# Performance work log

Hardware: AMD Instinct MI355X
Metric: run time of the kernel (lower is better)

## Reference

```python
import jax, jax.numpy as jnp
import numpy as np

# Hard-coded 36-node detector graph from the source (1-indexed), 220 directed edges.
E_SRC = [1,2,3,4,5,6,7,8,9,10,11,12,13,14,15,16,17,18,19,20,21,22,23,24,25,26,27,28,29,30,31,32,33,34,35,36,4,3,8,7,19,20,15,16,35,36,31,32,11,12,11,11,11,12,12,12,6,5,25,26,28,25,9,9,9,10,10,10,1,2,3,4,5,6,7,8,9,10,11,12,13,14,15,16,17,18,17,18,19,20,16,15,31,32,36,35,3,4,7,8,6,5,25,28,14,9,12,11,1,4,2,3,4,1,6,7,8,5,10,11,12,9,14,15,16,13,18,19,20,17,22,23,24,21,26,27,28,25,30,31,32,29,34,35,36,33,33,34,1,2,14,13,30,29,23,22,21,24,22,21,36,33,4,31,30,15,27,28,18,17,10,9,14,19,18,5,8,1,19,20,21,22,23,24,25,26,27,28,29,30,31,32,33,34,35,36,25,26,13,14,30,29,24,21,23,22,33,34,1,2,28,27,10,9,12,15,22,21,11,10]
E_DST = [2,3,4,1,6,7,8,5,10,11,12,9,14,15,16,13,18,19,20,17,22,23,24,21,26,27,28,25,30,31,32,29,34,35,36,33,33,34,1,2,14,13,30,29,23,22,21,24,22,21,36,33,4,31,30,15,27,28,18,17,10,9,14,19,18,5,8,1,19,20,21,22,23,24,25,26,27,28,29,30,31,32,33,34,35,36,25,26,13,14,30,29,24,21,23,22,33,34,1,2,28,27,10,9,12,15,22,21,11,10,1,2,3,4,5,6,7,8,9,10,11,12,13,14,15,16,17,18,19,20,21,22,23,24,25,26,27,28,29,30,31,32,33,34,35,36,4,3,8,7,19,20,15,16,35,36,31,32,11,12,11,11,11,12,12,12,6,5,25,26,28,25,9,9,9,10,10,10,1,2,3,4,5,6,7,8,9,10,11,12,13,14,15,16,17,18,17,18,19,20,16,15,31,32,36,35,3,4,7,8,6,5,25,28,14,9,12,11,1,4]

B = 20000   # graphs per batch
P = 36      # nodes per graph
N = B * P


def setup_inputs() -> dict:
    key = jax.random.key(0)
    ks = jax.random.split(key, 12)
    src = np.asarray(E_SRC, np.int32) - 1
    dst = np.asarray(E_DST, np.int32) - 1
    offs = (np.arange(B, dtype=np.int32) * P)[:, None]
    edge_index = jnp.asarray(np.stack([(src[None, :] + offs).reshape(-1),
                                       (dst[None, :] + offs).reshape(-1)]))  # [2, B*220]
    batch_index = jnp.asarray(np.repeat(np.arange(B, dtype=np.int32), P))  # [N]
    x = jax.random.normal(ks[0], (N, 2), jnp.float32)
    pos = jax.random.normal(ks[1], (N, 3), jnp.float32)  # unused by forward (faithful to source)

    def lin_w(k, fi, fo):
        s = 1.0 / np.sqrt(fi)
        return jax.random.uniform(k, (fi, fo), jnp.float32, -s, s)

    def lin_b(k, fo):
        return jax.random.uniform(k, (fo,), jnp.float32, -0.05, 0.05)

    return {
        "x": x, "edge_index": edge_index, "pos": pos, "batch_index": batch_index,
        "W0": lin_w(ks[2], 2, 4),   "b0": lin_b(ks[3], 4),
        "W1": lin_w(ks[4], 4, 12),  "b1": lin_b(ks[5], 12),
        "W2": lin_w(ks[6], 12, 16), "b2": lin_b(ks[7], 16),
        "W3": lin_w(ks[8], 16, 32), "b3": lin_b(ks[9], 32),
        "Wfc": lin_w(ks[10], 64, 7), "bfc": lin_b(ks[11], 7),
    }


def reference(x, edge_index, pos, batch_index, W0, b0, W1, b1, W2, b2, W3, b3, Wfc, bfc):
    del pos  # present in the torch signature but unused
    src, dst = edge_index[0], edge_index[1]
    n = x.shape[0]
    # GCN symmetric normalization with self-loops: deg = 1 + in-degree
    deg = jax.ops.segment_sum(jnp.ones(src.shape, x.dtype), dst, num_segments=n) + 1.0
    inv = deg ** -0.5
    enorm = inv[src] * inv[dst]   # edge norm
    snorm = inv * inv             # self-loop norm (deg^-1)

    def gcn_conv(h, W, b):
        h = h @ W  # [n, fo]
        agg = jax.ops.segment_sum(h[src] * enorm[:, None], dst, num_segments=n)
        return agg + h * snorm[:, None] + b

    h = jax.nn.relu(gcn_conv(x, W0, b0))
    h = jax.nn.relu(gcn_conv(h, W1, b1))
    # dropout(0.2) is identity in eval mode
    h = jax.nn.relu(gcn_conv(h, W2, b2))
    h = jax.nn.relu(gcn_conv(h, W3, b3))

    gmp = jax.ops.segment_max(h, batch_index, num_segments=B)
    counts = jax.ops.segment_sum(jnp.ones((n,), h.dtype), batch_index, num_segments=B)
    gap = jax.ops.segment_sum(h, batch_index, num_segments=B) / counts[:, None]
    hidden = jnp.concatenate([gmp, gap], axis=1)  # [B, 64]
    out = jax.nn.relu(hidden @ Wfc + bfc)         # [B, 7]
    return (out, hidden)
```

## Files before the change

kernel.cpp:

```cpp
#include <hip/hip_runtime.h>

typedef __attribute__((ext_vector_type(2))) float f32x2;
typedef __attribute__((ext_vector_type(4))) float f32x4;
typedef _Float16 f16;
typedef __attribute__((ext_vector_type(4))) _Float16 f16x4;
typedef __attribute__((ext_vector_type(8))) _Float16 f16x8;

#define NGRAPH 20000
#define GPB 7
#define STRIDE 36
#define SB (STRIDE * 4)

static __constant__ int c_indeg[36] = {
    7,5,5,7,6,5,5,6,9,9,9,9,5,7,7,5,5,6,6,5,7,7,5,5,7,5,5,7,5,6,6,5,6,5,5,6
};
static __constant__ signed char c_adj[36][9] = {
    {3,7,9,6,1,18,10,0,0},      {0,6,7,2,19,0,0,0,0},
    {1,3,33,32,20,0,0,0,0},     {2,10,0,32,21,33,9,0,0},
    {7,9,5,27,22,26,0,0,0},     {4,6,26,23,27,0,0,0,0},
    {5,7,1,24,0,0,0,0,0},       {6,9,4,0,25,1,0,0,0},
    {11,24,27,9,13,18,17,26,14},{8,27,24,3,10,4,7,0,27},
    {9,0,11,21,35,32,3,28,20},  {10,13,8,20,30,29,14,29,21},
    {15,19,18,13,30,0,0,0,0},   {12,18,8,19,14,31,11,0,0},
    {13,11,8,15,29,32,28,0,0},  {14,12,28,33,29,0,0,0,0},
    {19,25,17,34,24,0,0,0,0},   {16,24,8,18,35,25,0,0,0},
    {17,8,0,19,13,12,0,0,0},    {18,1,16,12,13,0,0,0,0},
    {23,30,11,2,31,10,21,0,0},  {20,35,10,3,34,11,22,0,0},
    {21,34,4,35,23,0,0,0,0},    {22,31,5,30,20,0,0,0,0},
    {27,6,16,25,17,8,9,0,0},    {24,7,17,26,16,0,0,0,0},
    {25,5,8,27,4,0,0,0,0},      {26,4,9,5,24,9,8,0,0},
    {31,15,10,14,29,0,0,0,0},   {28,14,11,11,15,30,0,0,0},
    {29,11,12,31,20,23,0,0,0},  {30,13,28,23,20,0,0,0,0},
    {35,3,10,14,2,33,0,0,0},    {32,2,15,3,34,0,0,0,0},
    {33,16,35,22,21,0,0,0,0},   {34,10,17,32,21,22,0,0,0},
};
static __constant__ float c_inv[36] = {
    0.35355339f,0.40824829f,0.40824829f,0.35355339f,0.37796447f,0.40824829f,
    0.40824829f,0.37796447f,0.31622777f,0.31622777f,0.31622777f,0.31622777f,
    0.40824829f,0.35355339f,0.35355339f,0.40824829f,0.40824829f,0.37796447f,
    0.37796447f,0.40824829f,0.35355339f,0.35355339f,0.40824829f,0.40824829f,
    0.35355339f,0.40824829f,0.40824829f,0.35355339f,0.40824829f,0.37796447f,
    0.37796447f,0.40824829f,0.37796447f,0.40824829f,0.40824829f,0.37796447f,
};
#define A_ 0.35355339f
#define B_ 0.40824829f
#define C_ 0.37796447f
#define D_ 0.31622777f
static __constant__ float c_ninv[36][9] = {
    {A_,C_,D_,B_,B_,C_,D_,0,0}, {A_,B_,C_,B_,B_,0,0,0,0},
    {B_,A_,B_,C_,A_,0,0,0,0},   {B_,D_,A_,C_,A_,B_,D_,0,0},
    {C_,D_,B_,A_,B_,B_,0,0,0},  {C_,B_,B_,B_,A_,0,0,0,0},
    {B_,C_,B_,A_,A_,0,0,0,0},   {B_,D_,C_,A_,B_,B_,0,0,0},
    {D_,A_,A_,D_,A_,C_,C_,B_,A_},{D_,A_,A_,A_,D_,C_,C_,A_,A_},
    {D_,A_,D_,A_,C_,C_,A_,B_,A_},{D_,A_,D_,A_,C_,C_,A_,C_,A_},
    {B_,B_,C_,A_,C_,0,0,0,0},   {B_,C_,D_,B_,A_,B_,D_,0,0},
    {A_,D_,D_,B_,C_,C_,B_,0,0}, {A_,B_,B_,B_,C_,0,0,0,0},
    {B_,B_,C_,B_,A_,0,0,0,0},   {B_,A_,D_,C_,C_,B_,0,0,0},
    {C_,D_,A_,B_,A_,B_,0,0,0},  {C_,B_,B_,B_,A_,0,0,0,0},
    {B_,C_,D_,B_,B_,D_,A_,0,0}, {A_,C_,D_,A_,B_,D_,B_,0,0},
    {A_,B_,C_,C_,B_,0,0,0,0},   {B_,B_,B_,C_,A_,0,0,0,0},
    {A_,B_,B_,B_,C_,D_,D_,0,0}, {A_,C_,C_,B_,B_,0,0,0,0},
    {B_,B_,D_,A_,C_,0,0,0,0},   {B_,C_,D_,B_,A_,D_,D_,0,0},
    {B_,B_,D_,A_,C_,0,0,0,0},   {B_,A_,D_,D_,B_,C_,0,0,0},
    {C_,D_,B_,B_,A_,B_,0,0,0},  {C_,A_,B_,B_,A_,0,0,0,0},
    {C_,A_,D_,A_,B_,B_,0,0,0},  {C_,B_,B_,A_,B_,0,0,0,0},
    {B_,B_,C_,B_,A_,0,0,0,0},   {B_,D_,C_,C_,A_,B_,0,0,0},
};

static __device__ __forceinline__ f32x2 relu2(f32x2 v) {
    return __builtin_elementwise_max(v, (f32x2){0.f, 0.f});
}

extern "C" __global__ __launch_bounds__(256, 4)
void gcn_fused(const float* __restrict__ x,
               const float* __restrict__ W0, const float* __restrict__ b0,
               const float* __restrict__ W1, const float* __restrict__ b1,
               const float* __restrict__ W2, const float* __restrict__ b2,
               const float* __restrict__ W3, const float* __restrict__ b3,
               const float* __restrict__ Wfc, const float* __restrict__ bfc,
               float* __restrict__ out)
{
    __shared__ float L[GPB * 36 * STRIDE];

    const int t = threadIdx.x;
    const int g = t / 36;
    const int v = t - g * 36;
    const bool act = (g < GPB);
    const int gq = act ? g : GPB - 1;
    const int vc = act ? v : 0;
    const int G  = blockIdx.x * GPB + g;
    const int Gc = (act && G < NGRAPH) ? G : 0;

    const int nd = c_indeg[vc];
    const float inv_v = c_inv[vc];
    const float* nr = &c_ninv[vc][0];
    int aoff[9];
#pragma unroll
    for (int k = 0; k < 9; ++k)
        aoff[k] = (gq * 36 + (int)c_adj[vc][k]) * SB;
    float* srow = &L[(gq * 36 + vc) * STRIDE];
    char* srowb = (char*)srow;
    const char* Lb = (const char*)L;

    f32x2 h0a, h0b;
    {
        const float2 xv = ((const float2*)x)[(size_t)Gc * 36 + vc];
        const float s0 = xv.x * inv_v, s1 = xv.y * inv_v;
        if (act) { srow[32] = s0; srow[33] = s1; }
        __syncthreads();
        f32x2 c = {s0, s1};
#pragma unroll
        for (int k = 0; k < 5; ++k) c += *(const f32x2*)(Lb + aoff[k] + 128);
        if (nd > 5) c += *(const f32x2*)(Lb + aoff[5] + 128);
        if (nd > 6) c += *(const f32x2*)(Lb + aoff[6] + 128);
        if (nd > 7) { c += *(const f32x2*)(Lb + aoff[7] + 128);
                      c += *(const f32x2*)(Lb + aoff[8] + 128); }
        const float a0 = c.x * inv_v, a1 = c.y * inv_v;
        const f32x2 a0v = {a0, a0}, a1v = {a1, a1};
        const f32x2* W0v = (const f32x2*)W0;
        const f32x2* b0v = (const f32x2*)b0;
        h0a = relu2(__builtin_elementwise_fma(a0v, W0v[0],
                    __builtin_elementwise_fma(a1v, W0v[2], b0v[0])));
        h0b = relu2(__builtin_elementwise_fma(a0v, W0v[1],
                    __builtin_elementwise_fma(a1v, W0v[3], b0v[1])));
    }

    f32x2 h1[6];
    {
        const f32x2 iv = {inv_v, inv_v};
        const f32x2 s0 = h0a * iv, s1 = h0b * iv;
        if (act) *(f32x4*)&srow[0] = (f32x4){s0.x, s0.y, s1.x, s1.y};
        __syncthreads();
        f32x4 c = {s0.x, s0.y, s1.x, s1.y};
#pragma unroll
        for (int k = 0; k < 5; ++k) c += *(const f32x4*)(Lb + aoff[k]);
        if (nd > 5) c += *(const f32x4*)(Lb + aoff[5]);
        if (nd > 6) c += *(const f32x4*)(Lb + aoff[6]);
        if (nd > 7) { c += *(const f32x4*)(Lb + aoff[7]);
                      c += *(const f32x4*)(Lb + aoff[8]); }
        float a[4];
#pragma unroll
        for (int i = 0; i < 4; ++i) a[i] = c[i] * inv_v;
        f32x2 z[6];
        const f32x2* b1v = (const f32x2*)b1;
#pragma unroll
        for (int j = 0; j < 6; ++j) z[j] = b1v[j];
        const f32x2* W1v = (const f32x2*)W1;
#pragma unroll
        for (int i = 0; i < 4; ++i) {
            const f32x2 av = {a[i], a[i]};
#pragma unroll
            for (int j = 0; j < 6; ++j)
                z[j] = __builtin_elementwise_fma(av, W1v[i * 6 + j], z[j]);
        }
#pragma unroll
        for (int j = 0; j < 6; ++j) h1[j] = relu2(z[j]);
    }

    f32x2 h2[8];
    {
        if (act) {
            f16x8 wlo; f16x4 whi;
#pragma unroll
            for (int j = 0; j < 4; ++j) {
                wlo[2*j]   = (f16)h1[j].x;
                wlo[2*j+1] = (f16)h1[j].y;
            }
#pragma unroll
            for (int j = 0; j < 2; ++j) {
                whi[2*j]   = (f16)h1[4+j].x;
                whi[2*j+1] = (f16)h1[4+j].y;
            }
            *(f16x8*)(srowb + 16) = wlo;
            *(f16x4*)(srowb + 32) = whi;
        }
        __syncthreads();
        float c[12];
#pragma unroll
        for (int j = 0; j < 6; ++j) {
            c[2*j]   = h1[j].x * inv_v;
            c[2*j+1] = h1[j].y * inv_v;
        }
#pragma unroll
        for (int k = 0; k < 9; ++k) {
            if (k >= 5) {
                if (k == 5 && nd <= 5) break;
                if (k == 6 && nd <= 6) break;
                if (k == 7 && nd <= 7) break;
            }
            const char* base = Lb + aoff[k];
            const f16x8 lo = *(const f16x8*)(base + 16);
            const f16x4 hi = *(const f16x4*)(base + 32);
            const float w = nr[k];
#pragma unroll
            for (int i = 0; i < 8; ++i) c[i]     = fmaf((float)lo[i], w, c[i]);
#pragma unroll
            for (int i = 0; i < 4; ++i) c[8 + i] = fmaf((float)hi[i], w, c[8 + i]);
        }
        float a[12];
#pragma unroll
        for (int i = 0; i < 12; ++i) a[i] = c[i] * inv_v;
        f32x2 z[8];
        const f32x2* b2v = (const f32x2*)b2;
#pragma unroll
        for (int j = 0; j < 8; ++j) z[j] = b2v[j];
        const f32x2* W2v = (const f32x2*)W2;
#pragma unroll
        for (int i = 0; i < 12; ++i) {
            const f32x2 av = {a[i], a[i]};
#pragma unroll
            for (int j = 0; j < 8; ++j)
                z[j] = __builtin_elementwise_fma(av, W2v[i * 8 + j], z[j]);
        }
#pragma unroll
        for (int j = 0; j < 8; ++j) h2[j] = relu2(z[j]);
    }

    f32x2 h3[16];
    {
        if (act) {
            f16x8 wlo, whi;
#pragma unroll
            for (int j = 0; j < 4; ++j) {
                wlo[2*j]   = (f16)h2[j].x;
                wlo[2*j+1] = (f16)h2[j].y;
                whi[2*j]   = (f16)h2[4+j].x;
                whi[2*j+1] = (f16)h2[4+j].y;
            }
            *(f16x8*)(srowb + 48) = wlo;
            *(f16x8*)(srowb + 64) = whi;
        }
        __syncthreads();
        float c[16];
#pragma unroll
        for (int j = 0; j < 8; ++j) {
            c[2*j]   = h2[j].x * inv_v;
            c[2*j+1] = h2[j].y * inv_v;
        }
#pragma unroll
        for (int k = 0; k < 9; ++k) {
            if (k >= 5) {
                if (k == 5 && nd <= 5) break;
                if (k == 6 && nd <= 6) break;
                if (k == 7 && nd <= 7) break;
            }
            const char* base = Lb + aoff[k];
            const f16x8 lo = *(const f16x8*)(base + 48);
            const f16x8 hi = *(const f16x8*)(base + 64);
            const float w = nr[k];
#pragma unroll
            for (int i = 0; i < 8; ++i) c[i]     = fmaf((float)lo[i], w, c[i]);
#pragma unroll
            for (int i = 0; i < 8; ++i) c[8 + i] = fmaf((float)hi[i], w, c[8 + i]);
        }
        float a[16];
#pragma unroll
        for (int i = 0; i < 16; ++i) a[i] = c[i] * inv_v;
        f32x2 z[16];
        const f32x2* b3v = (const f32x2*)b3;
#pragma unroll
        for (int j = 0; j < 16; ++j) z[j] = b3v[j];
        const f32x2* W3v = (const f32x2*)W3;
#pragma unroll
        for (int i = 0; i < 16; ++i) {
            const f32x2 av = {a[i], a[i]};
#pragma unroll
            for (int j = 0; j < 16; ++j)
                z[j] = __builtin_elementwise_fma(av, W3v[i * 16 + j], z[j]);
        }
#pragma unroll
        for (int j = 0; j < 16; ++j) h3[j] = relu2(z[j]);
    }

    if (act) {
        *(f32x4*)&srow[0] = (f32x4){h3[0].x, h3[0].y, h3[1].x, h3[1].y};
        *(f32x4*)&srow[4] = (f32x4){h3[2].x, h3[2].y, h3[3].x, h3[3].y};
        *(f32x4*)&srow[8] = (f32x4){h3[4].x, h3[4].y, h3[5].x, h3[5].y};
    }
    __syncthreads();
    if (act) {
#pragma unroll
        for (int q = 0; q < 5; ++q)
            *(f32x4*)&srow[12 + q * 4] =
                (f32x4){h3[6+2*q].x, h3[6+2*q].y, h3[7+2*q].x, h3[7+2*q].y};
    }
    __syncthreads();

    if (t < GPB * 32) {
        const int pg = t >> 5, pf = t & 31;
        const int PG = blockIdx.x * GPB + pg;
        const float* col = &L[(pg * 36) * STRIDE + pf];
        float mx = -1e30f, sm = 0.f;
#pragma unroll
        for (int u = 0; u < 36; ++u) {
            const float val = col[u * STRIDE];
            mx = fmaxf(mx, val); sm += val;
        }
        const float gap = sm * (1.0f / 36.0f);
        if (PG < NGRAPH) {
            float* ho = out + (size_t)NGRAPH * 7 + (size_t)PG * 64;
            ho[pf] = mx; ho[32 + pf] = gap;
        }
        float p[7];
        const float* wr0 = Wfc + pf * 7;
        const float* wr1 = Wfc + (32 + pf) * 7;
#pragma unroll
        for (int o = 0; o < 7; ++o)
            p[o] = fmaf(mx, wr0[o], gap * wr1[o]);
#pragma unroll
        for (int m = 16; m >= 1; m >>= 1) {
#pragma unroll
            for (int o = 0; o < 7; ++o)
                p[o] += __shfl_xor(p[o], m, 32);
        }
        if (pf < 7 && PG < NGRAPH) {
            float w = p[0];
            w = (pf == 1) ? p[1] : w;
            w = (pf == 2) ? p[2] : w;
            w = (pf == 3) ? p[3] : w;
            w = (pf == 4) ? p[4] : w;
            w = (pf == 5) ? p[5] : w;
            w = (pf == 6) ? p[6] : w;
            out[(size_t)PG * 7 + pf] = fmaxf(w + bfc[pf], 0.f);
        }
    }
}

extern "C" void kernel_launch(void* const* d_in, const int* in_sizes, int n_in,
                              void* d_out, int out_size, void* d_ws, size_t ws_size,
                              hipStream_t stream) {
    (void)in_sizes; (void)n_in; (void)d_ws; (void)ws_size; (void)out_size;
    const float* x   = (const float*)d_in[0];
    const float* W0  = (const float*)d_in[4];
    const float* b0  = (const float*)d_in[5];
    const float* W1  = (const float*)d_in[6];
    const float* b1  = (const float*)d_in[7];
    const float* W2  = (const float*)d_in[8];
    const float* b2  = (const float*)d_in[9];
    const float* W3  = (const float*)d_in[10];
    const float* b3  = (const float*)d_in[11];
    const float* Wfc = (const float*)d_in[12];
    const float* bfc = (const float*)d_in[13];
    float* out = (float*)d_out;

    const int nblocks = (NGRAPH + GPB - 1) / GPB;
    hipLaunchKernelGGL(gcn_fused, dim3(nblocks), dim3(256), 0, stream,
                       x, W0, b0, W1, b1, W2, b2, W3, b3, Wfc, bfc, out);
}
```

Before: 36.64 us.

## Gather layer-0 inputs from global memory, unroll aggregation, use LDS-based FC head

Layer 0 now reads neighbor features directly from global x instead of staging them in shared memory, which removes one barrier. Adjacency bytes are unpacked from packed words. The per-layer aggregation loops are replaced with explicit macro expansions guarded by in-degree. The final FC head is changed from a 7-way shuffle reduction to a staging pass: pooled features go to a small LDS region and 49 threads each compute one output dot product. This adds one barrier and extra LDS but removes the shuffle traffic.

```diff
diff --git a/kernel.cpp b/kernel.cpp
--- a/kernel.cpp
+++ b/kernel.cpp
@@ -10,6 +10,8 @@
 #define GPB 7
 #define STRIDE 36
 #define SB (STRIDE * 4)
+#define HID_OFF (GPB * 36 * STRIDE)
+#define HSTR 68
 
 static __constant__ int c_indeg[36] = {
     7,5,5,7,6,5,5,6,9,9,9,9,5,7,7,5,5,6,6,5,7,7,5,5,7,5,5,7,5,6,6,5,6,5,5,6
@@ -80,7 +82,7 @@
                const float* __restrict__ Wfc, const float* __restrict__ bfc,
                float* __restrict__ out)
 {
-    __shared__ float L[GPB * 36 * STRIDE];
+    __shared__ float L[GPB * 36 * STRIDE + GPB * HSTR];
 
     const int t = threadIdx.x;
     const int g = t / 36;
@@ -94,28 +96,47 @@
     const int nd = c_indeg[vc];
     const float inv_v = c_inv[vc];
     const float* nr = &c_ninv[vc][0];
-    int aoff[9];
-#pragma unroll
-    for (int k = 0; k < 9; ++k)
-        aoff[k] = (gq * 36 + (int)c_adj[vc][k]) * SB;
+    int nb[9], aoff[9];
+    {
+        const unsigned char* ar = (const unsigned char*)&c_adj[vc][0];
+        const unsigned int w0 = *(const unsigned int*)(ar);
+        const unsigned int w1 = *(const unsigned int*)(ar + 4);
+        const unsigned int w2 = *(const unsigned int*)(ar + 8);
+#pragma unroll
+        for (int k = 0; k < 4; ++k) nb[k] = (int)((w0 >> (8 * k)) & 0xff);
+#pragma unroll
+        for (int k = 0; k < 4; ++k) nb[4 + k] = (int)((w1 >> (8 * k)) & 0xff);
+        nb[8] = (int)(w2 & 0xff);
+#pragma unroll
+        for (int k = 0; k < 9; ++k) aoff[k] = (gq * 36 + nb[k]) * SB;
+    }
     float* srow = &L[(gq * 36 + vc) * STRIDE];
     char* srowb = (char*)srow;
     const char* Lb = (const char*)L;
 
     f32x2 h0a, h0b;
     {
-        const float2 xv = ((const float2*)x)[(size_t)Gc * 36 + vc];
-        const float s0 = xv.x * inv_v, s1 = xv.y * inv_v;
-        if (act) { srow[32] = s0; srow[33] = s1; }
-        __syncthreads();
-        f32x2 c = {s0, s1};
-#pragma unroll
-        for (int k = 0; k < 5; ++k) c += *(const f32x2*)(Lb + aoff[k] + 128);
-        if (nd > 5) c += *(const f32x2*)(Lb + aoff[5] + 128);
-        if (nd > 6) c += *(const f32x2*)(Lb + aoff[6] + 128);
-        if (nd > 7) { c += *(const f32x2*)(Lb + aoff[7] + 128);
-                      c += *(const f32x2*)(Lb + aoff[8] + 128); }
-        const float a0 = c.x * inv_v, a1 = c.y * inv_v;
+        const float2* x2 = (const float2*)x;
+        const int xb = Gc * 36;
+        const float2 xs = x2[xb + vc];
+        f32x2 acc = {xs.x * inv_v, xs.y * inv_v};
+#pragma unroll
+        for (int k = 0; k < 5; ++k) {
+            const float2 xu = x2[xb + nb[k]];
+            const float w = nr[k];
+            acc.x = fmaf(w, xu.x, acc.x); acc.y = fmaf(w, xu.y, acc.y);
+        }
+        if (nd > 5) { const float2 xu = x2[xb + nb[5]]; const float w = nr[5];
+            acc.x = fmaf(w, xu.x, acc.x); acc.y = fmaf(w, xu.y, acc.y); }
+        if (nd > 6) { const float2 xu = x2[xb + nb[6]]; const float w = nr[6];
+            acc.x = fmaf(w, xu.x, acc.x); acc.y = fmaf(w, xu.y, acc.y); }
+        if (nd > 7) {
+            const float2 xu7 = x2[xb + nb[7]]; const float w7 = nr[7];
+            acc.x = fmaf(w7, xu7.x, acc.x); acc.y = fmaf(w7, xu7.y, acc.y);
+            const float2 xu8 = x2[xb + nb[8]]; const float w8 = nr[8];
+            acc.x = fmaf(w8, xu8.x, acc.x); acc.y = fmaf(w8, xu8.y, acc.y);
+        }
+        const float a0 = acc.x * inv_v, a1 = acc.y * inv_v;
         const f32x2 a0v = {a0, a0}, a1v = {a1, a1};
         const f32x2* W0v = (const f32x2*)W0;
         const f32x2* b0v = (const f32x2*)b0;
@@ -181,22 +202,19 @@
             c[2*j]   = h1[j].x * inv_v;
             c[2*j+1] = h1[j].y * inv_v;
         }
-#pragma unroll
-        for (int k = 0; k < 9; ++k) {
-            if (k >= 5) {
-                if (k == 5 && nd <= 5) break;
-                if (k == 6 && nd <= 6) break;
-                if (k == 7 && nd <= 7) break;
-            }
-            const char* base = Lb + aoff[k];
-            const f16x8 lo = *(const f16x8*)(base + 16);
-            const f16x4 hi = *(const f16x4*)(base + 32);
-            const float w = nr[k];
-#pragma unroll
-            for (int i = 0; i < 8; ++i) c[i]     = fmaf((float)lo[i], w, c[i]);
-#pragma unroll
-            for (int i = 0; i < 4; ++i) c[8 + i] = fmaf((float)hi[i], w, c[8 + i]);
-        }
+#define AGG2(K) { const char* base = Lb + aoff[K];                              \
+        const f16x8 lo = *(const f16x8*)(base + 16);                            \
+        const f16x4 hi = *(const f16x4*)(base + 32);                            \
+        const float w = nr[K];                                                  \
+        _Pragma("unroll") for (int i = 0; i < 8; ++i)                           \
+            c[i] = fmaf((float)lo[i], w, c[i]);                                 \
+        _Pragma("unroll") for (int i = 0; i < 4; ++i)                           \
+            c[8+i] = fmaf((float)hi[i], w, c[8+i]); }
+        AGG2(0) AGG2(1) AGG2(2) AGG2(3) AGG2(4)
+        if (nd > 5) AGG2(5)
+        if (nd > 6) AGG2(6)
+        if (nd > 7) { AGG2(7) AGG2(8) }
+#undef AGG2
         float a[12];
 #pragma unroll
         for (int i = 0; i < 12; ++i) a[i] = c[i] * inv_v;
@@ -237,22 +255,19 @@
             c[2*j]   = h2[j].x * inv_v;
             c[2*j+1] = h2[j].y * inv_v;
         }
-#pragma unroll
-        for (int k = 0; k < 9; ++k) {
-            if (k >= 5) {
-                if (k == 5 && nd <= 5) break;
-                if (k == 6 && nd <= 6) break;
-                if (k == 7 && nd <= 7) break;
-            }
-            const char* base = Lb + aoff[k];
-            const f16x8 lo = *(const f16x8*)(base + 48);
-            const f16x8 hi = *(const f16x8*)(base + 64);
-            const float w = nr[k];
-#pragma unroll
-            for (int i = 0; i < 8; ++i) c[i]     = fmaf((float)lo[i], w, c[i]);
-#pragma unroll
-            for (int i = 0; i < 8; ++i) c[8 + i] = fmaf((float)hi[i], w, c[8 + i]);
-        }
+#define AGG3(K) { const char* base = Lb + aoff[K];                              \
+        const f16x8 lo = *(const f16x8*)(base + 48);                            \
+        const f16x8 hi = *(const f16x8*)(base + 64);                            \
+        const float w = nr[K];                                                  \
+        _Pragma("unroll") for (int i = 0; i < 8; ++i)                           \
+            c[i] = fmaf((float)lo[i], w, c[i]);                                 \
+        _Pragma("unroll") for (int i = 0; i < 8; ++i)                           \
+            c[8+i] = fmaf((float)hi[i], w, c[8+i]); }
+        AGG3(0) AGG3(1) AGG3(2) AGG3(3) AGG3(4)
+        if (nd > 5) AGG3(5)
+        if (nd > 6) AGG3(6)
+        if (nd > 7) { AGG3(7) AGG3(8) }
+#undef AGG3
         float a[16];
 #pragma unroll
         for (int i = 0; i < 16; ++i) a[i] = c[i] * inv_v;
@@ -286,6 +301,7 @@
     }
     __syncthreads();
 
+    float* hid = &L[HID_OFF];
     if (t < GPB * 32) {
         const int pg = t >> 5, pf = t & 31;
         const int PG = blockIdx.x * GPB + pg;
@@ -297,32 +313,27 @@
             mx = fmaxf(mx, val); sm += val;
         }
         const float gap = sm * (1.0f / 36.0f);
+        hid[pg * HSTR + pf] = mx;
+        hid[pg * HSTR + 32 + pf] = gap;
         if (PG < NGRAPH) {
             float* ho = out + (size_t)NGRAPH * 7 + (size_t)PG * 64;
             ho[pf] = mx; ho[32 + pf] = gap;
         }
-        float p[7];
-        const float* wr0 = Wfc + pf * 7;
-        const float* wr1 = Wfc + (32 + pf) * 7;
-#pragma unroll
-        for (int o = 0; o < 7; ++o)
-            p[o] = fmaf(mx, wr0[o], gap * wr1[o]);
-#pragma unroll
-        for (int m = 16; m >= 1; m >>= 1) {
-#pragma unroll
-            for (int o = 0; o < 7; ++o)
-                p[o] += __shfl_xor(p[o], m, 32);
-        }
-        if (pf < 7 && PG < NGRAPH) {
-            float w = p[0];
-            w = (pf == 1) ? p[1] : w;
-            w = (pf == 2) ? p[2] : w;
-            w = (pf == 3) ? p[3] : w;
-            w = (pf == 4) ? p[4] : w;
-            w = (pf == 5) ? p[5] : w;
-            w = (pf == 6) ? p[6] : w;
-            out[(size_t)PG * 7 + pf] = fmaxf(w + bfc[pf], 0.f);
-        }
+    }
+    __syncthreads();
+
+    if (t < GPB * 7) {
+        const int fg = t / 7, o = t - fg * 7;
+        float acc = bfc[o];
+        const float2* hh = (const float2*)&hid[fg * HSTR];
+#pragma unroll
+        for (int j = 0; j < 32; ++j) {
+            const float2 hp = hh[j];
+            acc = fmaf(hp.x, Wfc[(2*j) * 7 + o],
+                  fmaf(hp.y, Wfc[(2*j+1) * 7 + o], acc));
+        }
+        const int FG = blockIdx.x * GPB + fg;
+        if (FG < NGRAPH) out[(size_t)FG * 7 + o] = fmaxf(acc, 0.f);
     }
 }
 
```

Result: slower. 37.85 us (+3.3%).
